# Kernel tuning notes

Measured on AMD Instinct MI355X. Metric: run time of the kernel, lower is better.

The kernel has to match this reference:

```python
import jax, jax.numpy as jnp
import numpy as np

N_NODES = 50000
N_EDGES = 800000
D_IN = 128
K = 4  # num_kernels
F = 32  # out_feats


def setup_inputs() -> dict:
    key = jax.random.key(0)
    ks = jax.random.split(key, 6)
    feat = jax.random.normal(ks[0], (N_NODES, D_IN), dtype=jnp.float32)
    # fc weight [out=K*F, in=D_IN], xavier-normal-ish scale
    W = jax.random.normal(ks[1], (K * F, D_IN), dtype=jnp.float32) * np.float32(np.sqrt(2.0 / (K * F + D_IN)))
    bias = jnp.zeros((1, K, F), dtype=jnp.float32)
    mu = jax.random.normal(ks[2], (1, K, F), dtype=jnp.float32) * 0.1
    sigma = jax.random.uniform(ks[3], (K, 1), dtype=jnp.float32)
    src = jax.random.randint(ks[4], (N_EDGES,), 0, N_NODES, dtype=jnp.int32)
    dst = jax.random.randint(ks[5], (N_EDGES,), 0, N_NODES, dtype=jnp.int32)
    return {"feat": feat, "W": W, "bias": bias, "mu": mu, "sigma": sigma, "src": src, "dst": dst}


def reference(feat, W, bias, mu, sigma, src, dst):
    n = feat.shape[0]
    # fc projection: [N, D_in] @ [D_in, K*F] -> [N, K, F]
    ft = (feat @ W.T).reshape(n, K, F)
    ft_src = ft[src]  # [E, K, F]
    ft_dst = ft[dst]  # [E, K, F]
    # Gaussian kernel per edge: exp(-sigma_k * ||(ft_src - ft_dst) - mu||_2 over F)
    diff = ft_src - ft_dst - mu  # [E, K, F]
    knorm = jnp.sqrt(jnp.sum(diff * diff, axis=2, keepdims=True))  # [E, K, 1]
    logits = -knorm * sigma  # sigma [K,1] broadcasts -> [E, K, 1]
    # edge softmax over incoming edges of each destination node
    seg_max = jax.ops.segment_max(logits, dst, num_segments=n)  # [N, K, 1]
    e = jnp.exp(logits - seg_max[dst])
    seg_sum = jax.ops.segment_sum(e, dst, num_segments=n)  # [N, K, 1]
    a = e / seg_sum[dst]  # [E, K, 1]
    # message = u_mul_e, reduce = sum to dst
    msg = ft_src * a  # [E, K, F]
    rst = jax.ops.segment_sum(msg, dst, num_segments=n)  # [N, K, F]
    return rst + bias
```

## Files before the change

kernel.cpp:

```cpp
#include <hip/hip_runtime.h>
#include <math.h>

#define N_NODES 50000
#define N_EDGES 800000
#define NBUCKET 1563
#define NB_POW  2048
#define CAP     704
#define BIN     64
#define SPAD    72
#define SC_BLOCKS 196
#define GEMM_BLOCKS 782
#define SENT 0xFFFFFFFFu

typedef __attribute__((ext_vector_type(8))) short bf16x8;
typedef __attribute__((ext_vector_type(4))) float f32x4;

__device__ __forceinline__ unsigned short f2b(float f) {
    union { float f; unsigned u; } v; v.f = f;
    return (unsigned short)((v.u + 0x7FFFu + ((v.u >> 16) & 1u)) >> 16);
}
__device__ __forceinline__ float b2f_lo(unsigned u) {
    union { unsigned u; float f; } v; v.u = u << 16; return v.f;
}
__device__ __forceinline__ float b2f_hi(unsigned u) {
    union { unsigned u; float f; } v; v.u = u & 0xFFFF0000u; return v.f;
}
__device__ __forceinline__ void decode8(uint4 r, float* f) {
    f[0] = b2f_lo(r.x); f[1] = b2f_hi(r.x);
    f[2] = b2f_lo(r.y); f[3] = b2f_hi(r.y);
    f[4] = b2f_lo(r.z); f[5] = b2f_hi(r.z);
    f[6] = b2f_lo(r.w); f[7] = b2f_hi(r.w);
}

__global__ __launch_bounds__(256) void prep(const float* __restrict__ W,
                                            unsigned short* __restrict__ Wb,
                                            int* __restrict__ bcount) {
    int idx = blockIdx.x * 256 + threadIdx.x;
    if (idx < 4096) {
        int i = idx * 4;
        float4 v = *(const float4*)(W + i);
        Wb[i + 0] = f2b(v.x); Wb[i + 1] = f2b(v.y);
        Wb[i + 2] = f2b(v.z); Wb[i + 3] = f2b(v.w);
    } else if (idx < 4096 + NB_POW) {
        bcount[idx - 4096] = 0;
    }
}

__global__ __launch_bounds__(256) void produce(const float* __restrict__ feat,
                                               const unsigned short* __restrict__ Wb,
                                               unsigned short* __restrict__ ftb,
                                               const int* __restrict__ src,
                                               const int* __restrict__ dst,
                                               int* __restrict__ bcount,
                                               unsigned* __restrict__ pool, int n) {
    if (blockIdx.x < SC_BLOCKS) {
        __shared__ int hist[NB_POW];
        __shared__ int gbase[NB_POW];
        __shared__ int cur[NB_POW];
        int t = threadIdx.x;
        #pragma unroll
        for (int i = 0; i < NB_POW / 256; ++i) hist[t + i * 256] = 0;
        __syncthreads();

        unsigned key[16];
        int ebase = blockIdx.x * 4096 + (t << 2);
        #pragma unroll
        for (int i = 0; i < 4; ++i) {
            int e = ebase + i * 1024;
            if (e + 3 < N_EDGES) {
                int4 s4 = *(const int4*)(src + e);
                int4 d4 = *(const int4*)(dst + e);
                key[i * 4 + 0] = ((unsigned)d4.x << 16) | (unsigned)s4.x;
                key[i * 4 + 1] = ((unsigned)d4.y << 16) | (unsigned)s4.y;
                key[i * 4 + 2] = ((unsigned)d4.z << 16) | (unsigned)s4.z;
                key[i * 4 + 3] = ((unsigned)d4.w << 16) | (unsigned)s4.w;
            } else {
                #pragma unroll
                for (int j = 0; j < 4; ++j) {
                    int ee = e + j;
                    key[i * 4 + j] = (ee < N_EDGES)
                        ? (((unsigned)dst[ee] << 16) | (unsigned)src[ee]) : SENT;
                }
            }
        }
        #pragma unroll
        for (int i = 0; i < 16; ++i)
            if (key[i] != SENT) atomicAdd(&hist[key[i] >> 21], 1);
        __syncthreads();
        #pragma unroll
        for (int i = 0; i < NB_POW / 256; ++i) {
            int b = t + i * 256;
            int h = hist[b];
            cur[b] = 0;
            gbase[b] = (h > 0) ? atomicAdd(&bcount[b], h) : 0;
        }
        __syncthreads();
        #pragma unroll
        for (int i = 0; i < 16; ++i) {
            unsigned kk = key[i];
            if (kk != SENT) {
                int b = kk >> 21;
                int pos = gbase[b] + atomicAdd(&cur[b], 1);
                if (pos < CAP) pool[(size_t)b * CAP + pos] = kk;
            }
        }
        return;
    }
    int gb = blockIdx.x - SC_BLOCKS;
    int t = threadIdx.x;
    int wave = t >> 6, l = t & 63;
    int m = l & 15, quad = l >> 4;
    int row0 = gb * 64 + wave * 16;
    int grow = row0 + m;
    int arow = grow < n ? grow : (n - 1);
    f32x4 acc[8] = {};
    const float* ap = feat + (size_t)arow * 128 + quad * 8;
    #pragma unroll
    for (int ks = 0; ks < 4; ++ks) {
        float4 a0 = *(const float4*)(ap + ks * 32);
        float4 a1 = *(const float4*)(ap + ks * 32 + 4);
        bf16x8 af;
        af[0] = (short)f2b(a0.x); af[1] = (short)f2b(a0.y);
        af[2] = (short)f2b(a0.z); af[3] = (short)f2b(a0.w);
        af[4] = (short)f2b(a1.x); af[5] = (short)f2b(a1.y);
        af[6] = (short)f2b(a1.z); af[7] = (short)f2b(a1.w);
        #pragma unroll
        for (int ct = 0; ct < 8; ++ct) {
            int ncol = ct * 16 + m;
            bf16x8 bf = *(const bf16x8*)(Wb + (size_t)ncol * 128 + ks * 32 + quad * 8);
            acc[ct] = __builtin_amdgcn_mfma_f32_16x16x32_bf16(af, bf, acc[ct], 0, 0, 0);
        }
    }
    int orow = row0 + quad * 4;
    #pragma unroll
    for (int r = 0; r < 4; ++r) {
        int gr = orow + r;
        if (gr < n) {
            #pragma unroll
            for (int ct = 0; ct < 8; ++ct)
                ftb[(size_t)gr * 128 + ct * 16 + m] = f2b(acc[ct][r]);
        }
    }
}

__global__ __launch_bounds__(256) void fused_node(const unsigned short* __restrict__ ftb,
                                                  const float* __restrict__ mu,
                                                  const float* __restrict__ sigma,
                                                  const int* __restrict__ bcount,
                                                  const unsigned* __restrict__ pool,
                                                  const float* __restrict__ bias,
                                                  float* __restrict__ out, int n) {
    __shared__ unsigned short s_src[32][SPAD];
    __shared__ int dcnt[32];
    int t = threadIdx.x;
    int b = blockIdx.x;
    if (t < 32) dcnt[t] = 0;
    __syncthreads();
    int cnt = min(bcount[b], CAP);
    for (int i = t; i < cnt; i += 256) {
        unsigned kk = pool[(size_t)b * CAP + i];
        int dl = (kk >> 16) & 31;
        int slot = atomicAdd(&dcnt[dl], 1);
        if (slot < BIN) s_src[dl][slot] = (unsigned short)(kk & 0xFFFFu);
    }
    __syncthreads();

    int ng = t >> 4;
    int l8 = t & 15;
    int c8 = l8 << 3;
    int k = l8 >> 2;
    float sig = sigma[k];
    float4 m0 = *(const float4*)(mu + c8);
    float4 m1 = *(const float4*)(mu + c8 + 4);
    float4 bi0 = *(const float4*)(bias + c8);
    float4 bi1 = *(const float4*)(bias + c8 + 4);

    #pragma unroll
    for (int pass = 0; pass < 2; ++pass) {
        int dl = pass * 16 + ng;
        int node = b * 32 + dl;
        bool valid = node < n;
        int deg = valid ? min(dcnt[dl], BIN) : 0;

        float base[8];
        {
            uint4 d4 = make_uint4(0u, 0u, 0u, 0u);
            if (valid) d4 = *(const uint4*)(ftb + (size_t)node * 128 + c8);
            float bb[8];
            decode8(d4, bb);
            base[0] = bb[0] + m0.x; base[1] = bb[1] + m0.y;
            base[2] = bb[2] + m0.z; base[3] = bb[3] + m0.w;
            base[4] = bb[4] + m1.x; base[5] = bb[5] + m1.y;
            base[6] = bb[6] + m1.z; base[7] = bb[7] + m1.w;
        }

        float acc[8] = {};
        float den = 0.f;
        int j = 0;
        for (; j + 3 < deg; j += 4) {
            ushort4 ss = *(const ushort4*)&s_src[dl][j];
            uint4 r0 = *(const uint4*)(ftb + (size_t)ss.x * 128 + c8);
            uint4 r1 = *(const uint4*)(ftb + (size_t)ss.y * 128 + c8);
            uint4 r2 = *(const uint4*)(ftb + (size_t)ss.z * 128 + c8);
            uint4 r3 = *(const uint4*)(ftb + (size_t)ss.w * 128 + c8);
            float f0[8], f1[8], f2[8], f3[8];
            decode8(r0, f0); decode8(r1, f1); decode8(r2, f2); decode8(r3, f3);
            float q0 = 0.f, q1 = 0.f, q2 = 0.f, q3 = 0.f;
            #pragma unroll
            for (int i = 0; i < 8; ++i) {
                float d0 = f0[i] - base[i], d1 = f1[i] - base[i];
                float d2 = f2[i] - base[i], d3 = f3[i] - base[i];
                q0 = fmaf(d0, d0, q0); q1 = fmaf(d1, d1, q1);
                q2 = fmaf(d2, d2, q2); q3 = fmaf(d3, d3, q3);
            }
            q0 += __shfl_xor(q0, 1); q1 += __shfl_xor(q1, 1);
            q2 += __shfl_xor(q2, 1); q3 += __shfl_xor(q3, 1);
            q0 += __shfl_xor(q0, 2); q1 += __shfl_xor(q1, 2);
            q2 += __shfl_xor(q2, 2); q3 += __shfl_xor(q3, 2);
            float w0 = __expf(-sig * sqrtf(q0));
            float w1 = __expf(-sig * sqrtf(q1));
            float w2 = __expf(-sig * sqrtf(q2));
            float w3 = __expf(-sig * sqrtf(q3));
            #pragma unroll
            for (int i = 0; i < 8; ++i)
                acc[i] = fmaf(f0[i], w0, fmaf(f1[i], w1, fmaf(f2[i], w2, fmaf(f3[i], w3, acc[i]))));
            den += (w0 + w1) + (w2 + w3);
        }
        for (; j < deg; ++j) {
            int s0 = s_src[dl][j];
            uint4 r0 = *(const uint4*)(ftb + (size_t)s0 * 128 + c8);
            float f0[8];
            decode8(r0, f0);
            float q0 = 0.f;
            #pragma unroll
            for (int i = 0; i < 8; ++i) {
                float d0 = f0[i] - base[i];
                q0 = fmaf(d0, d0, q0);
            }
            q0 += __shfl_xor(q0, 1);
            q0 += __shfl_xor(q0, 2);
            float w0 = __expf(-sig * sqrtf(q0));
            #pragma unroll
            for (int i = 0; i < 8; ++i) acc[i] = fmaf(f0[i], w0, acc[i]);
            den += w0;
        }

        if (valid) {
            float inv = (deg > 0) ? 1.0f / den : 0.f;
            float4 o0, o1;
            o0.x = acc[0] * inv + bi0.x; o0.y = acc[1] * inv + bi0.y;
            o0.z = acc[2] * inv + bi0.z; o0.w = acc[3] * inv + bi0.w;
            o1.x = acc[4] * inv + bi1.x; o1.y = acc[5] * inv + bi1.y;
            o1.z = acc[6] * inv + bi1.z; o1.w = acc[7] * inv + bi1.w;
            *(float4*)(out + (size_t)node * 128 + c8) = o0;
            *(float4*)(out + (size_t)node * 128 + c8 + 4) = o1;
        }
    }
}

extern "C" void kernel_launch(void* const* d_in, const int* in_sizes, int n_in,
                              void* d_out, int out_size, void* d_ws, size_t ws_size,
                              hipStream_t stream) {
    const float* feat  = (const float*)d_in[0];
    const float* W     = (const float*)d_in[1];
    const float* bias  = (const float*)d_in[2];
    const float* mu    = (const float*)d_in[3];
    const float* sigma = (const float*)d_in[4];
    const int*   src   = (const int*)d_in[5];
    const int*   dst   = (const int*)d_in[6];
    float* out = (float*)d_out;

    unsigned short* ftb = (unsigned short*)d_ws;
    unsigned short* Wb  = ftb + (size_t)N_NODES * 128;
    int* bcount = (int*)(Wb + 16384);
    unsigned* pool = (unsigned*)(bcount + NB_POW);

    prep<<<24, 256, 0, stream>>>(W, Wb, bcount);
    produce<<<SC_BLOCKS + GEMM_BLOCKS, 256, 0, stream>>>(feat, Wb, ftb, src, dst,
                                                         bcount, pool, N_NODES);
    fused_node<<<NBUCKET, 256, 0, stream>>>(ftb, mu, sigma, bcount, pool,
                                            bias, out, N_NODES);
}
```

Measured before the change: 149.0 us.

## Split each node bucket across two blocks and unroll gather by eight

The fused_node kernel now launches two blocks per 32-node bucket, each handling 16 destination nodes in a single pass instead of two sequential passes. The edge loop issues eight row gathers per iteration before consuming them, and launch bounds request higher occupancy. The aim is more parallelism and memory-level parallelism to hide gather latency. In exchange, each bucket's pool is read twice and filtered by each half, and register pressure from eight in-flight loads may rise.

```diff
diff --git a/kernel.cpp b/kernel.cpp
--- a/kernel.cpp
+++ b/kernel.cpp
@@ -14,6 +14,7 @@
 
 typedef __attribute__((ext_vector_type(8))) short bf16x8;
 typedef __attribute__((ext_vector_type(4))) float f32x4;
+typedef __attribute__((ext_vector_type(8))) float f32x8;
 
 __device__ __forceinline__ unsigned short f2b(float f) {
     union { float f; unsigned u; } v; v.f = f;
@@ -25,11 +26,13 @@
 __device__ __forceinline__ float b2f_hi(unsigned u) {
     union { unsigned u; float f; } v; v.u = u & 0xFFFF0000u; return v.f;
 }
-__device__ __forceinline__ void decode8(uint4 r, float* f) {
+__device__ __forceinline__ f32x8 dec8(uint4 r) {
+    f32x8 f;
     f[0] = b2f_lo(r.x); f[1] = b2f_hi(r.x);
     f[2] = b2f_lo(r.y); f[3] = b2f_hi(r.y);
     f[4] = b2f_lo(r.z); f[5] = b2f_hi(r.z);
     f[6] = b2f_lo(r.w); f[7] = b2f_hi(r.w);
+    return f;
 }
 
 __global__ __launch_bounds__(256) void prep(const float* __restrict__ W,
@@ -143,25 +146,73 @@
     }
 }
 
-__global__ __launch_bounds__(256) void fused_node(const unsigned short* __restrict__ ftb,
-                                                  const float* __restrict__ mu,
-                                                  const float* __restrict__ sigma,
-                                                  const int* __restrict__ bcount,
-                                                  const unsigned* __restrict__ pool,
-                                                  const float* __restrict__ bias,
-                                                  float* __restrict__ out, int n) {
-    __shared__ unsigned short s_src[32][SPAD];
-    __shared__ int dcnt[32];
+__device__ __forceinline__ void consume4(uint4 r0, uint4 r1, uint4 r2, uint4 r3,
+                                         f32x8 base, float sig,
+                                         f32x8& acc, float& den) {
+    f32x8 f0 = dec8(r0), f1 = dec8(r1), f2 = dec8(r2), f3 = dec8(r3);
+    float q0 = 0.f, q1 = 0.f, q2 = 0.f, q3 = 0.f;
+    #pragma unroll
+    for (int i = 0; i < 8; ++i) {
+        float d0 = f0[i] - base[i], d1 = f1[i] - base[i];
+        float d2 = f2[i] - base[i], d3 = f3[i] - base[i];
+        q0 = fmaf(d0, d0, q0); q1 = fmaf(d1, d1, q1);
+        q2 = fmaf(d2, d2, q2); q3 = fmaf(d3, d3, q3);
+    }
+    q0 += __shfl_xor(q0, 1); q1 += __shfl_xor(q1, 1);
+    q2 += __shfl_xor(q2, 1); q3 += __shfl_xor(q3, 1);
+    q0 += __shfl_xor(q0, 2); q1 += __shfl_xor(q1, 2);
+    q2 += __shfl_xor(q2, 2); q3 += __shfl_xor(q3, 2);
+    float w0 = __expf(-sig * sqrtf(q0));
+    float w1 = __expf(-sig * sqrtf(q1));
+    float w2 = __expf(-sig * sqrtf(q2));
+    float w3 = __expf(-sig * sqrtf(q3));
+    #pragma unroll
+    for (int i = 0; i < 8; ++i)
+        acc[i] = fmaf(f0[i], w0, fmaf(f1[i], w1, fmaf(f2[i], w2, fmaf(f3[i], w3, acc[i]))));
+    den += (w0 + w1) + (w2 + w3);
+}
+
+__device__ __forceinline__ void consume1(uint4 r0, f32x8 base, float sig,
+                                         f32x8& acc, float& den) {
+    f32x8 f0 = dec8(r0);
+    float q0 = 0.f;
+    #pragma unroll
+    for (int i = 0; i < 8; ++i) {
+        float d0 = f0[i] - base[i];
+        q0 = fmaf(d0, d0, q0);
+    }
+    q0 += __shfl_xor(q0, 1);
+    q0 += __shfl_xor(q0, 2);
+    float w0 = __expf(-sig * sqrtf(q0));
+    #pragma unroll
+    for (int i = 0; i < 8; ++i) acc[i] = fmaf(f0[i], w0, acc[i]);
+    den += w0;
+}
+
+__global__ __launch_bounds__(256, 4) void fused_node(const unsigned short* __restrict__ ftb,
+                                                     const float* __restrict__ mu,
+                                                     const float* __restrict__ sigma,
+                                                     const int* __restrict__ bcount,
+                                                     const unsigned* __restrict__ pool,
+                                                     const float* __restrict__ bias,
+                                                     float* __restrict__ out, int n) {
+    __shared__ __align__(16) unsigned short s_src[16][SPAD];
+    __shared__ int dcnt[16];
     int t = threadIdx.x;
-    int b = blockIdx.x;
-    if (t < 32) dcnt[t] = 0;
+    int bid = blockIdx.x;
+    int b = bid >> 1;
+    unsigned hsel = ((unsigned)bid & 1u) << 4;
+    if (t < 16) dcnt[t] = 0;
     __syncthreads();
     int cnt = min(bcount[b], CAP);
     for (int i = t; i < cnt; i += 256) {
         unsigned kk = pool[(size_t)b * CAP + i];
-        int dl = (kk >> 16) & 31;
-        int slot = atomicAdd(&dcnt[dl], 1);
-        if (slot < BIN) s_src[dl][slot] = (unsigned short)(kk & 0xFFFFu);
+        unsigned dl = (kk >> 16) & 31u;
+        if ((dl & 16u) == hsel) {
+            int d = (int)(dl & 15u);
+            int slot = atomicAdd(&dcnt[d], 1);
+            if (slot < BIN) s_src[d][slot] = (unsigned short)kk;
+        }
     }
     __syncthreads();
 
@@ -170,91 +221,58 @@
     int c8 = l8 << 3;
     int k = l8 >> 2;
     float sig = sigma[k];
-    float4 m0 = *(const float4*)(mu + c8);
-    float4 m1 = *(const float4*)(mu + c8 + 4);
-    float4 bi0 = *(const float4*)(bias + c8);
-    float4 bi1 = *(const float4*)(bias + c8 + 4);
-
-    #pragma unroll
-    for (int pass = 0; pass < 2; ++pass) {
-        int dl = pass * 16 + ng;
-        int node = b * 32 + dl;
-        bool valid = node < n;
-        int deg = valid ? min(dcnt[dl], BIN) : 0;
-
-        float base[8];
-        {
-            uint4 d4 = make_uint4(0u, 0u, 0u, 0u);
-            if (valid) d4 = *(const uint4*)(ftb + (size_t)node * 128 + c8);
-            float bb[8];
-            decode8(d4, bb);
-            base[0] = bb[0] + m0.x; base[1] = bb[1] + m0.y;
-            base[2] = bb[2] + m0.z; base[3] = bb[3] + m0.w;
-            base[4] = bb[4] + m1.x; base[5] = bb[5] + m1.y;
-            base[6] = bb[6] + m1.z; base[7] = bb[7] + m1.w;
-        }
-
-        float acc[8] = {};
-        float den = 0.f;
-        int j = 0;
-        for (; j + 3 < deg; j += 4) {
-            ushort4 ss = *(const ushort4*)&s_src[dl][j];
-            uint4 r0 = *(const uint4*)(ftb + (size_t)ss.x * 128 + c8);
-            uint4 r1 = *(const uint4*)(ftb + (size_t)ss.y * 128 + c8);
-            uint4 r2 = *(const uint4*)(ftb + (size_t)ss.z * 128 + c8);
-            uint4 r3 = *(const uint4*)(ftb + (size_t)ss.w * 128 + c8);
-            float f0[8], f1[8], f2[8], f3[8];
-            decode8(r0, f0); decode8(r1, f1); decode8(r2, f2); decode8(r3, f3);
-            float q0 = 0.f, q1 = 0.f, q2 = 0.f, q3 = 0.f;
-            #pragma unroll
-            for (int i = 0; i < 8; ++i) {
-                float d0 = f0[i] - base[i], d1 = f1[i] - base[i];
-                float d2 = f2[i] - base[i], d3 = f3[i] - base[i];
-                q0 = fmaf(d0, d0, q0); q1 = fmaf(d1, d1, q1);
-                q2 = fmaf(d2, d2, q2); q3 = fmaf(d3, d3, q3);
-            }
-            q0 += __shfl_xor(q0, 1); q1 += __shfl_xor(q1, 1);
-            q2 += __shfl_xor(q2, 1); q3 += __shfl_xor(q3, 1);
-            q0 += __shfl_xor(q0, 2); q1 += __shfl_xor(q1, 2);
-            q2 += __shfl_xor(q2, 2); q3 += __shfl_xor(q3, 2);
-            float w0 = __expf(-sig * sqrtf(q0));
-            float w1 = __expf(-sig * sqrtf(q1));
-            float w2 = __expf(-sig * sqrtf(q2));
-            float w3 = __expf(-sig * sqrtf(q3));
-            #pragma unroll
-            for (int i = 0; i < 8; ++i)
-                acc[i] = fmaf(f0[i], w0, fmaf(f1[i], w1, fmaf(f2[i], w2, fmaf(f3[i], w3, acc[i]))));
-            den += (w0 + w1) + (w2 + w3);
-        }
-        for (; j < deg; ++j) {
-            int s0 = s_src[dl][j];
-            uint4 r0 = *(const uint4*)(ftb + (size_t)s0 * 128 + c8);
-            float f0[8];
-            decode8(r0, f0);
-            float q0 = 0.f;
-            #pragma unroll
-            for (int i = 0; i < 8; ++i) {
-                float d0 = f0[i] - base[i];
-                q0 = fmaf(d0, d0, q0);
-            }
-            q0 += __shfl_xor(q0, 1);
-            q0 += __shfl_xor(q0, 2);
-            float w0 = __expf(-sig * sqrtf(q0));
-            #pragma unroll
-            for (int i = 0; i < 8; ++i) acc[i] = fmaf(f0[i], w0, acc[i]);
-            den += w0;
-        }
-
-        if (valid) {
-            float inv = (deg > 0) ? 1.0f / den : 0.f;
-            float4 o0, o1;
-            o0.x = acc[0] * inv + bi0.x; o0.y = acc[1] * inv + bi0.y;
-            o0.z = acc[2] * inv + bi0.z; o0.w = acc[3] * inv + bi0.w;
-            o1.x = acc[4] * inv + bi1.x; o1.y = acc[5] * inv + bi1.y;
-            o1.z = acc[6] * inv + bi1.z; o1.w = acc[7] * inv + bi1.w;
-            *(float4*)(out + (size_t)node * 128 + c8) = o0;
-            *(float4*)(out + (size_t)node * 128 + c8 + 4) = o1;
-        }
+    f32x8 muv = *(const f32x8*)(mu + c8);
+    f32x8 biasv = *(const f32x8*)(bias + c8);
+
+    int node = (b << 5) + (int)hsel + ng;
+    bool valid = node < n;
+    int deg = valid ? min(dcnt[ng], BIN) : 0;
+
+    f32x8 base;
+    {
+        uint4 d4 = make_uint4(0u, 0u, 0u, 0u);
+        if (valid) d4 = *(const uint4*)(ftb + (size_t)node * 128 + c8);
+        base = dec8(d4) + muv;
+    }
+
+    f32x8 acc = (f32x8)(0.f);
+    float den = 0.f;
+    const unsigned short* srow = &s_src[ng][0];
+    int j = 0;
+    for (; j + 7 < deg; j += 8) {
+        ushort4 sa = *(const ushort4*)(srow + j);
+        ushort4 sb = *(const ushort4*)(srow + j + 4);
+        uint4 r0 = *(const uint4*)(ftb + (((unsigned)sa.x << 7) + c8));
+        uint4 r1 = *(const uint4*)(ftb + (((unsigned)sa.y << 7) + c8));
+        uint4 r2 = *(const uint4*)(ftb + (((unsigned)sa.z << 7) + c8));
+        uint4 r3 = *(const uint4*)(ftb + (((unsigned)sa.w << 7) + c8));
+        uint4 r4 = *(const uint4*)(ftb + (((unsigned)sb.x << 7) + c8));
+        uint4 r5 = *(const uint4*)(ftb + (((unsigned)sb.y << 7) + c8));
+        uint4 r6 = *(const uint4*)(ftb + (((unsigned)sb.z << 7) + c8));
+        uint4 r7 = *(const uint4*)(ftb + (((unsigned)sb.w << 7) + c8));
+        consume4(r0, r1, r2, r3, base, sig, acc, den);
+        consume4(r4, r5, r6, r7, base, sig, acc, den);
+    }
+    if (j + 3 < deg) {
+        ushort4 sa = *(const ushort4*)(srow + j);
+        uint4 r0 = *(const uint4*)(ftb + (((unsigned)sa.x << 7) + c8));
+        uint4 r1 = *(const uint4*)(ftb + (((unsigned)sa.y << 7) + c8));
+        uint4 r2 = *(const uint4*)(ftb + (((unsigned)sa.z << 7) + c8));
+        uint4 r3 = *(const uint4*)(ftb + (((unsigned)sa.w << 7) + c8));
+        consume4(r0, r1, r2, r3, base, sig, acc, den);
+        j += 4;
+    }
+    for (; j < deg; ++j) {
+        uint4 r0 = *(const uint4*)(ftb + (((unsigned)srow[j] << 7) + c8));
+        consume1(r0, base, sig, acc, den);
+    }
+
+    if (valid) {
+        float inv = (deg > 0) ? 1.0f / den : 0.f;
+        f32x8 o;
+        #pragma unroll
+        for (int i = 0; i < 8; ++i) o[i] = fmaf(acc[i], inv, biasv[i]);
+        *(f32x8*)(out + (size_t)node * 128 + c8) = o;
     }
 }
 
@@ -278,6 +296,6 @@
     prep<<<24, 256, 0, stream>>>(W, Wb, bcount);
     produce<<<SC_BLOCKS + GEMM_BLOCKS, 256, 0, stream>>>(feat, Wb, ftb, src, dst,
                                                          bcount, pool, N_NODES);
-    fused_node<<<NBUCKET, 256, 0, stream>>>(ftb, mu, sigma, bcount, pool,
-                                            bias, out, N_NODES);
-}
+    fused_node<<<2 * NBUCKET, 256, 0, stream>>>(ftb, mu, sigma, bcount, pool,
+                                                bias, out, N_NODES);
+}
```

Measured after the change: 153.0 us. 2.7% more time.

## Interleave two destination nodes per thread group with batched masked gathers

Applied to the files above, without the earlier changes.

The fused_node kernel now processes both destination nodes of a thread group together instead of in two sequential passes. It issues eight independent gather loads per iteration behind a scheduling barrier to raise memory-level parallelism. Tail handling moves from a scalar remainder loop to masked weights over zero-initialised source slots, and exp/sqrt use exp2 with a prescaled sigma and a raw hardware sqrt. It adds a launch-bounds occupancy hint, at the cost of more registers and wasted work on padded slots when the two nodes' degrees differ.

```diff
diff --git a/kernel.cpp b/kernel.cpp
--- a/kernel.cpp
+++ b/kernel.cpp
@@ -14,6 +14,7 @@
 
 typedef __attribute__((ext_vector_type(8))) short bf16x8;
 typedef __attribute__((ext_vector_type(4))) float f32x4;
+typedef __attribute__((ext_vector_type(8))) float f32x8;
 
 __device__ __forceinline__ unsigned short f2b(float f) {
     union { float f; unsigned u; } v; v.f = f;
@@ -25,11 +26,13 @@
 __device__ __forceinline__ float b2f_hi(unsigned u) {
     union { unsigned u; float f; } v; v.u = u & 0xFFFF0000u; return v.f;
 }
-__device__ __forceinline__ void decode8(uint4 r, float* f) {
+__device__ __forceinline__ f32x8 dec8(uint4 r) {
+    f32x8 f;
     f[0] = b2f_lo(r.x); f[1] = b2f_hi(r.x);
     f[2] = b2f_lo(r.y); f[3] = b2f_hi(r.y);
     f[4] = b2f_lo(r.z); f[5] = b2f_hi(r.z);
     f[6] = b2f_lo(r.w); f[7] = b2f_hi(r.w);
+    return f;
 }
 
 __global__ __launch_bounds__(256) void prep(const float* __restrict__ W,
@@ -143,17 +146,55 @@
     }
 }
 
-__global__ __launch_bounds__(256) void fused_node(const unsigned short* __restrict__ ftb,
-                                                  const float* __restrict__ mu,
-                                                  const float* __restrict__ sigma,
-                                                  const int* __restrict__ bcount,
-                                                  const unsigned* __restrict__ pool,
-                                                  const float* __restrict__ bias,
-                                                  float* __restrict__ out, int n) {
-    __shared__ unsigned short s_src[32][SPAD];
+__device__ __forceinline__ void consume4m(uint4 r0, uint4 r1, uint4 r2, uint4 r3,
+                                          f32x8 base, float nsig2, int rem,
+                                          f32x8& acc, float& den) {
+    f32x8 f0 = dec8(r0), f1 = dec8(r1), f2 = dec8(r2), f3 = dec8(r3);
+    float q0 = 0.f, q1 = 0.f, q2 = 0.f, q3 = 0.f;
+    #pragma unroll
+    for (int i = 0; i < 8; ++i) {
+        float d0 = f0[i] - base[i], d1 = f1[i] - base[i];
+        float d2 = f2[i] - base[i], d3 = f3[i] - base[i];
+        q0 = fmaf(d0, d0, q0); q1 = fmaf(d1, d1, q1);
+        q2 = fmaf(d2, d2, q2); q3 = fmaf(d3, d3, q3);
+    }
+    q0 += __shfl_xor(q0, 1); q1 += __shfl_xor(q1, 1);
+    q2 += __shfl_xor(q2, 1); q3 += __shfl_xor(q3, 1);
+    q0 += __shfl_xor(q0, 2); q1 += __shfl_xor(q1, 2);
+    q2 += __shfl_xor(q2, 2); q3 += __shfl_xor(q3, 2);
+    float w0 = exp2f(nsig2 * __builtin_amdgcn_sqrtf(q0));
+    float w1 = exp2f(nsig2 * __builtin_amdgcn_sqrtf(q1));
+    float w2 = exp2f(nsig2 * __builtin_amdgcn_sqrtf(q2));
+    float w3 = exp2f(nsig2 * __builtin_amdgcn_sqrtf(q3));
+    w0 = (rem > 0) ? w0 : 0.f;
+    w1 = (rem > 1) ? w1 : 0.f;
+    w2 = (rem > 2) ? w2 : 0.f;
+    w3 = (rem > 3) ? w3 : 0.f;
+    #pragma unroll
+    for (int i = 0; i < 8; ++i)
+        acc[i] = fmaf(f0[i], w0, fmaf(f1[i], w1, fmaf(f2[i], w2, fmaf(f3[i], w3, acc[i]))));
+    den += (w0 + w1) + (w2 + w3);
+}
+
+__global__ __launch_bounds__(256, 4) void fused_node(const unsigned short* __restrict__ ftb,
+                                                     const float* __restrict__ mu,
+                                                     const float* __restrict__ sigma,
+                                                     const int* __restrict__ bcount,
+                                                     const unsigned* __restrict__ pool,
+                                                     const float* __restrict__ bias,
+                                                     float* __restrict__ out, int n) {
+    __shared__ __align__(16) unsigned short s_src[32][SPAD];
     __shared__ int dcnt[32];
     int t = threadIdx.x;
     int b = blockIdx.x;
+    {
+        uint4* p = (uint4*)&s_src[0][0];
+        #pragma unroll
+        for (int i = 0; i < 2; ++i) {
+            int idx = t + i * 256;
+            if (idx < 32 * SPAD * 2 / 16) p[idx] = make_uint4(0u, 0u, 0u, 0u);
+        }
+    }
     if (t < 32) dcnt[t] = 0;
     __syncthreads();
     int cnt = min(bcount[b], CAP);
@@ -161,100 +202,67 @@
         unsigned kk = pool[(size_t)b * CAP + i];
         int dl = (kk >> 16) & 31;
         int slot = atomicAdd(&dcnt[dl], 1);
-        if (slot < BIN) s_src[dl][slot] = (unsigned short)(kk & 0xFFFFu);
+        if (slot < BIN) s_src[dl][slot] = (unsigned short)kk;
     }
     __syncthreads();
 
     int ng = t >> 4;
     int l8 = t & 15;
     int c8 = l8 << 3;
-    int k = l8 >> 2;
-    float sig = sigma[k];
-    float4 m0 = *(const float4*)(mu + c8);
-    float4 m1 = *(const float4*)(mu + c8 + 4);
-    float4 bi0 = *(const float4*)(bias + c8);
-    float4 bi1 = *(const float4*)(bias + c8 + 4);
-
-    #pragma unroll
-    for (int pass = 0; pass < 2; ++pass) {
-        int dl = pass * 16 + ng;
-        int node = b * 32 + dl;
-        bool valid = node < n;
-        int deg = valid ? min(dcnt[dl], BIN) : 0;
-
-        float base[8];
-        {
-            uint4 d4 = make_uint4(0u, 0u, 0u, 0u);
-            if (valid) d4 = *(const uint4*)(ftb + (size_t)node * 128 + c8);
-            float bb[8];
-            decode8(d4, bb);
-            base[0] = bb[0] + m0.x; base[1] = bb[1] + m0.y;
-            base[2] = bb[2] + m0.z; base[3] = bb[3] + m0.w;
-            base[4] = bb[4] + m1.x; base[5] = bb[5] + m1.y;
-            base[6] = bb[6] + m1.z; base[7] = bb[7] + m1.w;
-        }
-
-        float acc[8] = {};
-        float den = 0.f;
-        int j = 0;
-        for (; j + 3 < deg; j += 4) {
-            ushort4 ss = *(const ushort4*)&s_src[dl][j];
-            uint4 r0 = *(const uint4*)(ftb + (size_t)ss.x * 128 + c8);
-            uint4 r1 = *(const uint4*)(ftb + (size_t)ss.y * 128 + c8);
-            uint4 r2 = *(const uint4*)(ftb + (size_t)ss.z * 128 + c8);
-            uint4 r3 = *(const uint4*)(ftb + (size_t)ss.w * 128 + c8);
-            float f0[8], f1[8], f2[8], f3[8];
-            decode8(r0, f0); decode8(r1, f1); decode8(r2, f2); decode8(r3, f3);
-            float q0 = 0.f, q1 = 0.f, q2 = 0.f, q3 = 0.f;
-            #pragma unroll
-            for (int i = 0; i < 8; ++i) {
-                float d0 = f0[i] - base[i], d1 = f1[i] - base[i];
-                float d2 = f2[i] - base[i], d3 = f3[i] - base[i];
-                q0 = fmaf(d0, d0, q0); q1 = fmaf(d1, d1, q1);
-                q2 = fmaf(d2, d2, q2); q3 = fmaf(d3, d3, q3);
-            }
-            q0 += __shfl_xor(q0, 1); q1 += __shfl_xor(q1, 1);
-            q2 += __shfl_xor(q2, 1); q3 += __shfl_xor(q3, 1);
-            q0 += __shfl_xor(q0, 2); q1 += __shfl_xor(q1, 2);
-            q2 += __shfl_xor(q2, 2); q3 += __shfl_xor(q3, 2);
-            float w0 = __expf(-sig * sqrtf(q0));
-            float w1 = __expf(-sig * sqrtf(q1));
-            float w2 = __expf(-sig * sqrtf(q2));
-            float w3 = __expf(-sig * sqrtf(q3));
-            #pragma unroll
-            for (int i = 0; i < 8; ++i)
-                acc[i] = fmaf(f0[i], w0, fmaf(f1[i], w1, fmaf(f2[i], w2, fmaf(f3[i], w3, acc[i]))));
-            den += (w0 + w1) + (w2 + w3);
-        }
-        for (; j < deg; ++j) {
-            int s0 = s_src[dl][j];
-            uint4 r0 = *(const uint4*)(ftb + (size_t)s0 * 128 + c8);
-            float f0[8];
-            decode8(r0, f0);
-            float q0 = 0.f;
-            #pragma unroll
-            for (int i = 0; i < 8; ++i) {
-                float d0 = f0[i] - base[i];
-                q0 = fmaf(d0, d0, q0);
-            }
-            q0 += __shfl_xor(q0, 1);
-            q0 += __shfl_xor(q0, 2);
-            float w0 = __expf(-sig * sqrtf(q0));
-            #pragma unroll
-            for (int i = 0; i < 8; ++i) acc[i] = fmaf(f0[i], w0, acc[i]);
-            den += w0;
-        }
-
-        if (valid) {
-            float inv = (deg > 0) ? 1.0f / den : 0.f;
-            float4 o0, o1;
-            o0.x = acc[0] * inv + bi0.x; o0.y = acc[1] * inv + bi0.y;
-            o0.z = acc[2] * inv + bi0.z; o0.w = acc[3] * inv + bi0.w;
-            o1.x = acc[4] * inv + bi1.x; o1.y = acc[5] * inv + bi1.y;
-            o1.z = acc[6] * inv + bi1.z; o1.w = acc[7] * inv + bi1.w;
-            *(float4*)(out + (size_t)node * 128 + c8) = o0;
-            *(float4*)(out + (size_t)node * 128 + c8 + 4) = o1;
-        }
+    float nsig2 = -sigma[l8 >> 2] * 1.4426950408889634f;
+    f32x8 muv = *(const f32x8*)(mu + c8);
+
+    int nodeA = (b << 5) + ng;
+    int nodeB = nodeA + 16;
+    bool vA = nodeA < n, vB = nodeB < n;
+    int degA = vA ? min(dcnt[ng], BIN) : 0;
+    int degB = vB ? min(dcnt[ng + 16], BIN) : 0;
+
+    f32x8 baseA, baseB;
+    {
+        uint4 dA = make_uint4(0u, 0u, 0u, 0u), dB = make_uint4(0u, 0u, 0u, 0u);
+        if (vA) dA = *(const uint4*)(ftb + (size_t)nodeA * 128 + c8);
+        if (vB) dB = *(const uint4*)(ftb + (size_t)nodeB * 128 + c8);
+        baseA = dec8(dA) + muv;
+        baseB = dec8(dB) + muv;
+    }
+
+    f32x8 accA = (f32x8)(0.f), accB = (f32x8)(0.f);
+    float denA = 0.f, denB = 0.f;
+    const unsigned short* rowA = &s_src[ng][0];
+    const unsigned short* rowB = &s_src[ng + 16][0];
+    int jmax = max(degA, degB);
+
+    for (int j = 0; j < jmax; j += 4) {
+        ushort4 sa = *(const ushort4*)(rowA + j);
+        ushort4 sb = *(const ushort4*)(rowB + j);
+        uint4 a0 = *(const uint4*)(ftb + (((unsigned)sa.x << 7) + c8));
+        uint4 a1 = *(const uint4*)(ftb + (((unsigned)sa.y << 7) + c8));
+        uint4 a2 = *(const uint4*)(ftb + (((unsigned)sa.z << 7) + c8));
+        uint4 a3 = *(const uint4*)(ftb + (((unsigned)sa.w << 7) + c8));
+        uint4 b0 = *(const uint4*)(ftb + (((unsigned)sb.x << 7) + c8));
+        uint4 b1 = *(const uint4*)(ftb + (((unsigned)sb.y << 7) + c8));
+        uint4 b2 = *(const uint4*)(ftb + (((unsigned)sb.z << 7) + c8));
+        uint4 b3 = *(const uint4*)(ftb + (((unsigned)sb.w << 7) + c8));
+        __builtin_amdgcn_sched_barrier(0);
+        consume4m(a0, a1, a2, a3, baseA, nsig2, degA - j, accA, denA);
+        consume4m(b0, b1, b2, b3, baseB, nsig2, degB - j, accB, denB);
+    }
+
+    f32x8 biasv = *(const f32x8*)(bias + c8);
+    if (vA) {
+        float inv = (degA > 0) ? 1.0f / denA : 0.f;
+        f32x8 o;
+        #pragma unroll
+        for (int i = 0; i < 8; ++i) o[i] = fmaf(accA[i], inv, biasv[i]);
+        *(f32x8*)(out + (size_t)nodeA * 128 + c8) = o;
+    }
+    if (vB) {
+        float inv = (degB > 0) ? 1.0f / denB : 0.f;
+        f32x8 o;
+        #pragma unroll
+        for (int i = 0; i < 8; ++i) o[i] = fmaf(accB[i], inv, biasv[i]);
+        *(f32x8*)(out + (size_t)nodeB * 128 + c8) = o;
     }
 }
 
```

After: 147.7 us. About the same (-0.8%).
